# Performance work log

Measured on AMD Instinct MI355X. Metric: run time of the kernel, lower is better.

## Reference

```python
import jax, jax.numpy as jnp
import numpy as np

D_MODEL = 1024
D_STATE = 16
D_CONV = 4
EXPAND = 2
D_INNER = D_MODEL * EXPAND          # 2048
DT_RANK = max(1, D_MODEL // 16)     # 64
BATCH, SEQ = 4, 2048


def setup_inputs() -> dict:
    key = jax.random.key(0)
    ks = jax.random.split(key, 8)
    s = lambda n: 1.0 / np.sqrt(n)
    x = jax.random.normal(ks[0], (BATCH, SEQ, D_MODEL), jnp.float32)
    in_proj_w = jax.random.normal(ks[1], (2 * D_INNER, D_MODEL), jnp.float32) * s(D_MODEL)
    conv_w = jax.random.normal(ks[2], (D_INNER, 1, D_CONV), jnp.float32) * s(D_CONV)
    conv_b = jax.random.normal(ks[3], (D_INNER,), jnp.float32) * 0.01
    x_proj_w = jax.random.normal(ks[4], (DT_RANK + 2 * D_STATE, D_INNER), jnp.float32) * s(D_INNER)
    dt_proj_w = jax.random.normal(ks[5], (D_INNER, DT_RANK), jnp.float32) * s(DT_RANK)
    dt_proj_b = jax.random.normal(ks[6], (D_INNER,), jnp.float32) * 0.01
    A_log = jnp.broadcast_to(jnp.log(jnp.arange(1, D_STATE + 1, dtype=jnp.float32))[None, :],
                             (D_INNER, D_STATE)).copy()
    D_param = jnp.ones((D_INNER,), jnp.float32)
    out_proj_w = jax.random.normal(ks[7], (D_MODEL, D_INNER), jnp.float32) * s(D_INNER)
    return {"x": x, "in_proj_w": in_proj_w, "conv_w": conv_w, "conv_b": conv_b,
            "x_proj_w": x_proj_w, "dt_proj_w": dt_proj_w, "dt_proj_b": dt_proj_b,
            "A_log": A_log, "D_param": D_param, "out_proj_w": out_proj_w}


def _ssm_forward(x, in_proj_w, conv_w, conv_b, x_proj_w, dt_proj_w, dt_proj_b,
                 A_log, D_param, out_proj_w):
    B, L, _ = x.shape
    # input projection -> (B, L, 2*D_INNER), split into x_ssm and gate z
    xz = jnp.einsum('bld,ed->ble', x, in_proj_w)
    x_ssm, z = xz[..., :D_INNER], xz[..., D_INNER:]
    # causal depthwise conv1d (torch pads both sides then slices [:L] == left pad only)
    xc = jnp.transpose(x_ssm, (0, 2, 1))  # (B, D_INNER, L)
    xc = jax.lax.conv_general_dilated(
        xc, conv_w, window_strides=(1,), padding=[(D_CONV - 1, 0)],
        dimension_numbers=('NCH', 'OIH', 'NCH'), feature_group_count=D_INNER)
    xc = xc + conv_b[None, :, None]
    x_ssm = jax.nn.silu(jnp.transpose(xc, (0, 2, 1)))  # (B, L, D_INNER)
    # input-dependent dt, B, C
    dbl = jnp.einsum('bld,ed->ble', x_ssm, x_proj_w)  # (B, L, DT_RANK+2N)
    dt_x = dbl[..., :DT_RANK]
    B_x = dbl[..., DT_RANK:DT_RANK + D_STATE]
    C_x = dbl[..., DT_RANK + D_STATE:]
    dt = jax.nn.softplus(jnp.einsum('blr,dr->bld', dt_x, dt_proj_w) + dt_proj_b)  # (B, L, D_INNER)
    A = -jnp.exp(A_log)  # (D_INNER, D_STATE)

    # selective scan over L with lax.scan; carry h: (B, D_INNER, D_STATE)
    def step(h, inp):
        dt_t, B_t, C_t, x_t = inp  # (B,D), (B,N), (B,N), (B,D)
        dA = jnp.exp(dt_t[:, :, None] * A[None, :, :])          # (B, D, N)
        dB = dt_t[:, :, None] * B_t[:, None, :]                 # (B, D, N)
        h = dA * h + dB * x_t[:, :, None]
        y_t = jnp.einsum('bdn,bn->bd', h, C_t)
        return h, y_t

    h0 = jnp.zeros((B, D_INNER, D_STATE), x.dtype)
    xs = (jnp.moveaxis(dt, 1, 0), jnp.moveaxis(B_x, 1, 0),
          jnp.moveaxis(C_x, 1, 0), jnp.moveaxis(x_ssm, 1, 0))
    _, ys = jax.lax.scan(step, h0, xs)          # ys: (L, B, D_INNER)
    y = jnp.moveaxis(ys, 0, 1) + D_param[None, None, :] * x_ssm
    y = y * jax.nn.silu(z)
    return jnp.einsum('ble,de->bld', y, out_proj_w)


def reference(x, in_proj_w, conv_w, conv_b, x_proj_w, dt_proj_w, dt_proj_b,
              A_log, D_param, out_proj_w):
    return _ssm_forward(x, in_proj_w, conv_w, conv_b, x_proj_w, dt_proj_w,
                        dt_proj_b, A_log, D_param, out_proj_w)
```

## Files before the change

kernel.cpp:

```cpp
#include <hip/hip_runtime.h>
#include <hip/hip_bf16.h>
#include <math.h>

#define D_MODEL 1024
#define D_STATE 16
#define D_CONV 4
#define D_INNER 2048
#define DT_RANK 64
#define BATCH 4
#define SEQ 2048
#define ML (BATCH * SEQ)
#define NCH 64
#define LOG_NCH 6
#define CL (SEQ / NCH)

typedef __attribute__((ext_vector_type(8))) short short8;
typedef __attribute__((ext_vector_type(8))) unsigned short u16x8;
typedef __attribute__((ext_vector_type(4))) float f32x4;

__device__ __forceinline__ float bf2f(unsigned short u) {
  union { unsigned int i; float f; } v;
  v.i = ((unsigned int)u) << 16;
  return v.f;
}
__device__ __forceinline__ unsigned short f2bf(float f) {
  union { float f; unsigned int i; } u;
  u.f = f;
  unsigned int r = u.i + 0x7fffu + ((u.i >> 16) & 1u);
  return (unsigned short)(r >> 16);
}
__device__ __forceinline__ unsigned int f2bf_pk(float a, float b) {
  union { __hip_bfloat162 h; unsigned int u; } cv;
  cv.h = __float22bfloat162_rn(make_float2(a, b));
  return cv.u;
}
template <bool BF>
__device__ __forceinline__ float ld1(const void* p, size_t i) {
  if constexpr (BF) return bf2f(((const unsigned short*)p)[i]);
  else return ((const float*)p)[i];
}
template <bool BF>
__device__ __forceinline__ void ld4(const void* p, size_t i, float o[4]) {
  if constexpr (BF) {
    ushort4 v = *(const ushort4*)((const unsigned short*)p + i);
    o[0] = bf2f(v.x); o[1] = bf2f(v.y); o[2] = bf2f(v.z); o[3] = bf2f(v.w);
  } else {
    float4 v = *(const float4*)((const float*)p + i);
    o[0] = v.x; o[1] = v.y; o[2] = v.z; o[3] = v.w;
  }
}

__device__ __forceinline__ void gl_lds16(const unsigned short* g,
                                         unsigned short* l) {
  __builtin_amdgcn_global_load_lds(
      (const __attribute__((address_space(1))) void*)g,
      (__attribute__((address_space(3))) void*)l, 16, 0, 0);
}

#define CVT_N0 (ML * 1024)
#define CVT_N1 (4096 * 1024)
#define CVT_N2 (1024 * 2048)
#define CVT_N3 (2048 * 64)
#define CVT_N4 (128 * 2048)
#define CVT_E0 CVT_N0
#define CVT_E1 (CVT_E0 + CVT_N1)
#define CVT_E2 (CVT_E1 + CVT_N2)
#define CVT_E3 (CVT_E2 + CVT_N3)
#define CVT_E4 (CVT_E3 + CVT_N4)

__device__ __forceinline__ void cvt4(const void* in, size_t i,
                                     unsigned short* out, size_t o, int bf) {
  if (bf) {
    *(ushort4*)(out + o) = *(const ushort4*)((const unsigned short*)in + i);
  } else {
    float4 f = *(const float4*)((const float*)in + i);
    uint2 v;
    v.x = f2bf_pk(f.x, f.y);
    v.y = f2bf_pk(f.z, f.w);
    *(uint2*)(out + o) = v;
  }
}

__global__ __launch_bounds__(256) void cvt_all_kernel(
    const void* __restrict__ x, const void* __restrict__ ipw,
    const void* __restrict__ opw, const void* __restrict__ dtw,
    const void* __restrict__ xpw, unsigned short* __restrict__ x_bf,
    unsigned short* __restrict__ ipw_bf, unsigned short* __restrict__ opw_bf,
    unsigned short* __restrict__ dtw_bf, unsigned short* __restrict__ xpw_pad,
    int* __restrict__ flag) {
  __shared__ int cnt;
  if (threadIdx.x == 0) cnt = 0;
  __syncthreads();
  {
    const unsigned int wv = ((const unsigned int*)x)[threadIdx.x];
    const unsigned int e = (wv >> 7) & 0xffu;
    if (e < 100u || e > 145u) atomicAdd(&cnt, 1);
  }
  __syncthreads();
  const int bf = (cnt < 32) ? 1 : 0;
  if (blockIdx.x == 0 && threadIdx.x == 0) flag[0] = bf;

  const size_t g = (size_t)(blockIdx.x * 256 + threadIdx.x) * 4;
  if (g < CVT_E0) {
    cvt4(x, g, x_bf, g, bf);
  } else if (g < CVT_E1) {
    const size_t i = g - CVT_E0;
    cvt4(ipw, i, ipw_bf, i, bf);
  } else if (g < CVT_E2) {
    const size_t i = g - CVT_E1;
    cvt4(opw, i, opw_bf, i, bf);
  } else if (g < CVT_E3) {
    const size_t i = g - CVT_E2;
    cvt4(dtw, i, dtw_bf, i, bf);
  } else if (g < CVT_E4) {
    const size_t i = g - CVT_E3;
    const int row = (int)(i >> 11);
    if (row < 96) {
      cvt4(xpw, i, xpw_pad, i, bf);
    } else {
      ushort4 z = {0, 0, 0, 0};
      *(ushort4*)(xpw_pad + i) = z;
    }
  }
}

#define K1_LDA 1024
#define K1_NT 16

#define K1_STG(srcbase, lds, t_, h_)                                       \
  {                                                                        \
    const unsigned short* s_ =                                             \
        (srcbase) + (size_t)(h_) * (128 * K1_LDA) + (size_t)(t_) * 64;     \
    unsigned short* d_ = (lds) + (((t_) & 1) * 2 + (h_)) * 8192 + w * 512; \
    gl_lds16(s_, d_);                                                      \
    gl_lds16(s_ + 64 * K1_LDA, d_ + 4096);                                 \
  }

__global__ __launch_bounds__(512, 2) void gemm256_k1(
    const unsigned short* __restrict__ A,
    const unsigned short* __restrict__ B,
    unsigned short* __restrict__ C) {
  __shared__ unsigned short As[32768];
  __shared__ unsigned short Bs[32768];
  const int tid = threadIdx.x;
  const int l = tid & 63, w = tid >> 6;
  const int bid = blockIdx.x;
  const int swz = (bid & 7) * 64 + (bid >> 3);
  const int m0 = (swz >> 4) * 256, n0 = (swz & 15) * 256;
  const int row0 = tid >> 3;
  const int c0 = (tid & 7) ^ (row0 & 7);
  const unsigned short* aSrc = A + (size_t)(m0 + row0) * K1_LDA + c0 * 8;
  const unsigned short* bSrc = B + (size_t)(n0 + row0) * K1_LDA + c0 * 8;
  const int q = l >> 4, mr = l & 15;
  const int wm = w >> 2, wn = w & 3;

  K1_STG(aSrc, As, 0, 0);
  K1_STG(aSrc, As, 0, 1);
  K1_STG(bSrc, Bs, 0, 0);
  K1_STG(bSrc, Bs, 0, 1);
  K1_STG(bSrc, Bs, 1, 0);
  K1_STG(bSrc, Bs, 1, 1);
  K1_STG(aSrc, As, 1, 0);
  asm volatile("s_waitcnt vmcnt(6)" ::: "memory");
  asm volatile("s_barrier" ::: "memory");

  f32x4 acc[8][4] = {};
  for (int t = 0; t < K1_NT; ++t) {
    const int tb = (t & 1) * 2;
    short8 bfr[4][2];
#pragma unroll
    for (int ni = 0; ni < 4; ++ni)
#pragma unroll
      for (int kk = 0; kk < 2; ++kk) {
        const int r = (wn & 1) * 64 + ni * 16 + mr;
        const int c = kk * 4 + q;
        bfr[ni][kk] = *(const short8*)&Bs[(tb + (wn >> 1)) * 8192 + r * 64 +
                                          ((c ^ (r & 7)) * 8)];
      }
#pragma unroll
    for (int p = 0; p < 4; ++p) {
      short8 af[2][2];
#pragma unroll
      for (int i = 0; i < 2; ++i)
#pragma unroll
        for (int kk = 0; kk < 2; ++kk) {
          const int r = (2 * p + i) * 16 + mr;
          const int c = kk * 4 + q;
          af[i][kk] = *(const short8*)&As[(tb + wm) * 8192 + r * 64 +
                                          ((c ^ (r & 7)) * 8)];
        }
      if (p == 0) {
        if (t + 1 < K1_NT) K1_STG(aSrc, As, t + 1, 1);
      } else if (p == 1) {
        if (t + 2 < K1_NT) K1_STG(bSrc, Bs, t + 2, 0);
      } else if (p == 2) {
        if (t + 2 < K1_NT) K1_STG(bSrc, Bs, t + 2, 1);
      } else {
        if (t + 2 < K1_NT) K1_STG(aSrc, As, t + 2, 0);
      }
      asm volatile("s_barrier" ::: "memory");
      __builtin_amdgcn_s_setprio(1);
#pragma unroll
      for (int i = 0; i < 2; ++i)
#pragma unroll
        for (int ni = 0; ni < 4; ++ni)
#pragma unroll
          for (int kk = 0; kk < 2; ++kk)
            acc[2 * p + i][ni] = __builtin_amdgcn_mfma_f32_16x16x32_bf16(
                af[i][kk], bfr[ni][kk], acc[2 * p + i][ni], 0, 0, 0);
      __builtin_amdgcn_s_setprio(0);
      if (p == 3) {
        if (t + 2 < K1_NT) {
          asm volatile("s_waitcnt vmcnt(6)" ::: "memory");
        } else {
          asm volatile("s_waitcnt vmcnt(0)" ::: "memory");
        }
      }
      asm volatile("s_barrier" ::: "memory");
    }
  }
#pragma unroll
  for (int mi = 0; mi < 8; ++mi) {
#pragma unroll
    for (int ni = 0; ni < 4; ++ni) {
      const int row = m0 + wm * 128 + mi * 16 + q * 4;
      const int col = n0 + wn * 64 + ni * 16 + mr;
      const size_t off0 = (size_t)row * 4096 + col;
      const unsigned int p01 = f2bf_pk(acc[mi][ni][0], acc[mi][ni][1]);
      const unsigned int p23 = f2bf_pk(acc[mi][ni][2], acc[mi][ni][3]);
      C[off0] = (unsigned short)p01;
      C[off0 + 4096] = (unsigned short)(p01 >> 16);
      C[off0 + 2 * 4096] = (unsigned short)p23;
      C[off0 + 3 * 4096] = (unsigned short)(p23 >> 16);
    }
  }
}

#define K6_LDA 2048
#define K6_NT 32

#define K6_STGA(t_, h_)                                                 \
  {                                                                     \
    const unsigned short* s_ =                                          \
        aSrc + (size_t)(h_) * (128 * K6_LDA) + (size_t)(t_) * 64;       \
    unsigned short* d_ = As + (((t_) & 1) * 2 + (h_)) * 8192 + w * 512; \
    gl_lds16(s_, d_);                                                   \
    gl_lds16(s_ + 64 * K6_LDA, d_ + 4096);                              \
  }
#define K6_STGB(t_)                                            \
  {                                                            \
    const unsigned short* s_ = bSrc + (size_t)(t_) * 64;       \
    unsigned short* d_ = Bs6 + ((t_) & 1) * 8192 + w * 512;    \
    gl_lds16(s_, d_);                                          \
    gl_lds16(s_ + 64 * K6_LDA, d_ + 4096);                     \
  }

__global__ __launch_bounds__(512, 2) void gemm256x128_k6(
    const unsigned short* __restrict__ A,
    const unsigned short* __restrict__ B,
    void* __restrict__ C,
    const int* __restrict__ flag) {
  __shared__ unsigned short As[32768];
  __shared__ unsigned short Bs6[16384];
  const int tid = threadIdx.x;
  const int l = tid & 63, w = tid >> 6;
  const int bid = blockIdx.x;
  const int swz = (bid & 7) * 32 + (bid >> 3);
  const int n0 = (swz & 7) * 128, m0 = (swz >> 3) * 256;
  const int row0 = tid >> 3;
  const int c0 = (tid & 7) ^ (row0 & 7);
  const unsigned short* aSrc = A + (size_t)(m0 + row0) * K6_LDA + c0 * 8;
  const unsigned short* bSrc = B + (size_t)(n0 + row0) * K6_LDA + c0 * 8;
  const int q = l >> 4, mr = l & 15;
  const int wm = w >> 2, wn = w & 3;

  K6_STGA(0, 0);
  K6_STGA(0, 1);
  K6_STGB(0);
  K6_STGB(1);
  K6_STGA(1, 0);
  asm volatile("s_waitcnt vmcnt(4)" ::: "memory");
  asm volatile("s_barrier" ::: "memory");

  f32x4 acc[8][2] = {};
  for (int t = 0; t < K6_NT; ++t) {
    const int tb = (t & 1) * 2;
    short8 bfr[2][2];
#pragma unroll
    for (int ni = 0; ni < 2; ++ni)
#pragma unroll
      for (int kk = 0; kk < 2; ++kk) {
        const int r = wn * 32 + ni * 16 + mr;
        const int c = kk * 4 + q;
        bfr[ni][kk] = *(const short8*)&Bs6[(t & 1) * 8192 + r * 64 +
                                           ((c ^ (r & 7)) * 8)];
      }
#pragma unroll
    for (int p = 0; p < 4; ++p) {
      short8 af[2][2];
#pragma unroll
      for (int i = 0; i < 2; ++i)
#pragma unroll
        for (int kk = 0; kk < 2; ++kk) {
          const int r = (2 * p + i) * 16 + mr;
          const int c = kk * 4 + q;
          af[i][kk] = *(const short8*)&As[(tb + wm) * 8192 + r * 64 +
                                          ((c ^ (r & 7)) * 8)];
        }
      if (p == 0) {
        if (t + 1 < K6_NT) K6_STGA(t + 1, 1);
      } else if (p == 1) {
        if (t + 2 < K6_NT) K6_STGB(t + 2);
      } else if (p == 3) {
        if (t + 2 < K6_NT) K6_STGA(t + 2, 0);
      }
      asm volatile("s_barrier" ::: "memory");
      __builtin_amdgcn_s_setprio(1);
#pragma unroll
      for (int i = 0; i < 2; ++i)
#pragma unroll
        for (int ni = 0; ni < 2; ++ni)
#pragma unroll
          for (int kk = 0; kk < 2; ++kk)
            acc[2 * p + i][ni] = __builtin_amdgcn_mfma_f32_16x16x32_bf16(
                af[i][kk], bfr[ni][kk], acc[2 * p + i][ni], 0, 0, 0);
      __builtin_amdgcn_s_setprio(0);
      if (p == 3) {
        if (t + 2 < K6_NT) {
          asm volatile("s_waitcnt vmcnt(4)" ::: "memory");
        } else {
          asm volatile("s_waitcnt vmcnt(0)" ::: "memory");
        }
      }
      asm volatile("s_barrier" ::: "memory");
    }
  }
  const int bf = *flag;
#pragma unroll
  for (int mi = 0; mi < 8; ++mi) {
#pragma unroll
    for (int ni = 0; ni < 2; ++ni) {
      const int row = m0 + wm * 128 + mi * 16 + q * 4;
      const int col = n0 + wn * 32 + ni * 16 + mr;
      const size_t off0 = (size_t)row * 1024 + col;
      if (bf) {
        const unsigned int p01 = f2bf_pk(acc[mi][ni][0], acc[mi][ni][1]);
        const unsigned int p23 = f2bf_pk(acc[mi][ni][2], acc[mi][ni][3]);
        unsigned short* C16 = (unsigned short*)C;
        C16[off0] = (unsigned short)p01;
        C16[off0 + 1024] = (unsigned short)(p01 >> 16);
        C16[off0 + 2 * 1024] = (unsigned short)p23;
        C16[off0 + 3 * 1024] = (unsigned short)(p23 >> 16);
      } else {
        float* Cf = (float*)C;
#pragma unroll
        for (int j = 0; j < 4; ++j)
          Cf[off0 + (size_t)j * 1024] = acc[mi][ni][j];
      }
    }
  }
}

template <int EPI, int TAG>
__global__ __launch_bounds__(256) void gemm_mfma(
    const unsigned short* __restrict__ Ain, int lda,
    const unsigned short* __restrict__ Bin, int ldb, void* __restrict__ C,
    int ldc, int K, const void* __restrict__ bias,
    const int* __restrict__ flag) {
  __shared__ unsigned short As[128 * 32];
  __shared__ unsigned short Bs[128 * 32];
  const unsigned short* A = Ain;
  const unsigned short* B = Bin;
  if (EPI == 3) {
    A += (size_t)blockIdx.z * 512;
    B += (size_t)blockIdx.z * 512;
  }
  const int tid = threadIdx.x;
  const int l = tid & 63, w = tid >> 6;
  const int bm = blockIdx.y * 128;
  const int bn = blockIdx.x * 128;
  const int r0 = w * 16 + (l >> 2);
  const int cc = (((l & 3) ^ ((l >> 2) & 3) ^ ((l >> 4) & 3))) * 8;
  const unsigned short* Ap0 = A + (size_t)(bm + r0) * lda + cc;
  const unsigned short* Ap1 = A + (size_t)(bm + r0 + 64) * lda + cc;
  const unsigned short* Bp0 = B + (size_t)(bn + r0) * ldb + cc;
  const unsigned short* Bp1 = B + (size_t)(bn + r0 + 64) * ldb + cc;
  const int q = l >> 4, mr = l & 15;
  const int wm = w >> 1, wn = w & 1;
  const int slot = (q ^ (mr & 3) ^ (mr >> 2)) * 8;
  f32x4 acc[4][4] = {};
  for (int k0 = 0; k0 < K; k0 += 32) {
    gl_lds16(Ap0 + k0, As + w * 512);
    gl_lds16(Ap1 + k0, As + 2048 + w * 512);
    gl_lds16(Bp0 + k0, Bs + w * 512);
    gl_lds16(Bp1 + k0, Bs + 2048 + w * 512);
    __syncthreads();
    short8 af[4], bfr[4];
#pragma unroll
    for (int mi = 0; mi < 4; ++mi)
      af[mi] = *(const short8*)&As[(wm * 64 + mi * 16 + mr) * 32 + slot];
#pragma unroll
    for (int ni = 0; ni < 4; ++ni)
      bfr[ni] = *(const short8*)&Bs[(wn * 64 + ni * 16 + mr) * 32 + slot];
#pragma unroll
    for (int mi = 0; mi < 4; ++mi)
#pragma unroll
      for (int ni = 0; ni < 4; ++ni)
        acc[mi][ni] = __builtin_amdgcn_mfma_f32_16x16x32_bf16(
            af[mi], bfr[ni], acc[mi][ni], 0, 0, 0);
    __syncthreads();
  }
  float* Cp3 = (EPI == 3)
                   ? ((float*)C + (size_t)blockIdx.z * ML * 128)
                   : (float*)C;
#pragma unroll
  for (int mi = 0; mi < 4; ++mi) {
#pragma unroll
    for (int ni = 0; ni < 4; ++ni) {
      const int row = bm + wm * 64 + mi * 16 + q * 4;
      const int col = bn + wn * 64 + ni * 16 + mr;
      const size_t off0 = (size_t)row * ldc + col;
      if (EPI == 3) {
#pragma unroll
        for (int j = 0; j < 4; ++j)
          Cp3[off0 + (size_t)j * ldc] = acc[mi][ni][j];
      } else {
        const unsigned int p01 = f2bf_pk(acc[mi][ni][0], acc[mi][ni][1]);
        const unsigned int p23 = f2bf_pk(acc[mi][ni][2], acc[mi][ni][3]);
        unsigned short* C16 = (unsigned short*)C;
        C16[off0] = (unsigned short)p01;
        C16[off0 + ldc] = (unsigned short)(p01 >> 16);
        C16[off0 + 2 * (size_t)ldc] = (unsigned short)p23;
        C16[off0 + 3 * (size_t)ldc] = (unsigned short)(p23 >> 16);
      }
    }
  }
}

__global__ __launch_bounds__(256) void reduceK3_kernel(
    const float* __restrict__ part, unsigned short* __restrict__ dbl) {
  const size_t i = (size_t)(blockIdx.x * 256 + threadIdx.x) * 4;
  const size_t st = (size_t)ML * 128;
  float4 a = *(const float4*)(part + i);
  float4 b = *(const float4*)(part + st + i);
  float4 c = *(const float4*)(part + 2 * st + i);
  float4 d = *(const float4*)(part + 3 * st + i);
  uint2 v;
  v.x = f2bf_pk(a.x + b.x + c.x + d.x, a.y + b.y + c.y + d.y);
  v.y = f2bf_pk(a.z + b.z + c.z + d.z, a.w + b.w + c.w + d.w);
  *(uint2*)(dbl + i) = v;
}

__global__ __launch_bounds__(256) void dt_gemm_kernel(
    const unsigned short* __restrict__ Adbl,
    const unsigned short* __restrict__ Bw,
    unsigned short* __restrict__ Cdt,
    const void* __restrict__ bias, const int* __restrict__ flag) {
  __shared__ unsigned short Bs[128 * 64];
  __shared__ unsigned short Ass[4][128 * 64];
  const int tid = threadIdx.x;
  const int l = tid & 63, w = tid >> 6;
  const int bn = blockIdx.x * 128;
  const int mg = blockIdx.y * 512;
  const int srow = tid >> 3;
  const int sc = ((tid & 7) ^ (srow & 7)) * 8;
  const unsigned short* aSrc = Adbl + (size_t)(mg + srow) * 128 + sc;
  const unsigned short* bSrc = Bw + (size_t)(bn + srow) * 64 + sc;
#define K4_STGB(i_) gl_lds16(bSrc + (i_) * 32 * 64, Bs + (i_)*2048 + w * 512)
#define K4_STGA(mt_, i_)                                  \
  gl_lds16(aSrc + (size_t)((mt_)*128 + (i_)*32) * 128,    \
           Ass[(mt_) & 3] + (i_)*2048 + w * 512)
  K4_STGB(0); K4_STGB(1); K4_STGB(2); K4_STGB(3);
  K4_STGA(0, 0); K4_STGA(0, 1); K4_STGA(0, 2); K4_STGA(0, 3);
  K4_STGA(1, 0); K4_STGA(1, 1); K4_STGA(1, 2); K4_STGA(1, 3);
  asm volatile("s_waitcnt vmcnt(4)" ::: "memory");
  asm volatile("s_barrier" ::: "memory");
  const int q = l >> 4, mr = l & 15;
  const int wm = w >> 1, wn = w & 1;
  short8 bfr[4][2];
#pragma unroll
  for (int ni = 0; ni < 4; ++ni)
#pragma unroll
    for (int kk = 0; kk < 2; ++kk) {
      const int r = wn * 64 + ni * 16 + mr;
      const int c = kk * 4 + q;
      bfr[ni][kk] = *(const short8*)&Bs[r * 64 + ((c ^ (r & 7)) * 8)];
    }
  const int bf = *flag;
  float bv[4];
#pragma unroll
  for (int ni = 0; ni < 4; ++ni) {
    const int col = bn + wn * 64 + ni * 16 + mr;
    bv[ni] = bf ? ld1<true>(bias, col) : ld1<false>(bias, col);
  }
#pragma unroll
  for (int mt = 0; mt < 4; ++mt) {
    if (mt + 2 < 4) {
      K4_STGA(mt + 2, 0); K4_STGA(mt + 2, 1);
      K4_STGA(mt + 2, 2); K4_STGA(mt + 2, 3);
    }
    short8 af[4][2];
#pragma unroll
    for (int mi = 0; mi < 4; ++mi)
#pragma unroll
      for (int kk = 0; kk < 2; ++kk) {
        const int r = wm * 64 + mi * 16 + mr;
        const int c = kk * 4 + q;
        af[mi][kk] =
            *(const short8*)&Ass[mt & 3][r * 64 + ((c ^ (r & 7)) * 8)];
      }
    f32x4 acc[4][4] = {};
#pragma unroll
    for (int mi = 0; mi < 4; ++mi)
#pragma unroll
      for (int ni = 0; ni < 4; ++ni)
#pragma unroll
        for (int kk = 0; kk < 2; ++kk)
          acc[mi][ni] = __builtin_amdgcn_mfma_f32_16x16x32_bf16(
              af[mi][kk], bfr[ni][kk], acc[mi][ni], 0, 0, 0);
#pragma unroll
    for (int mi = 0; mi < 4; ++mi) {
#pragma unroll
      for (int ni = 0; ni < 4; ++ni) {
        const int row = mg + mt * 128 + wm * 64 + mi * 16 + q * 4;
        const int col = bn + wn * 64 + ni * 16 + mr;
        const size_t off0 = (size_t)row * 4096 + col;
        float v[4];
#pragma unroll
        for (int j = 0; j < 4; ++j) {
          const float t = acc[mi][ni][j] + bv[ni];
          v[j] = fmaxf(t, 0.f) + __logf(1.f + __expf(-fabsf(t)));
        }
        const unsigned int p01 = f2bf_pk(v[0], v[1]);
        const unsigned int p23 = f2bf_pk(v[2], v[3]);
        Cdt[off0] = (unsigned short)p01;
        Cdt[off0 + 4096] = (unsigned short)(p01 >> 16);
        Cdt[off0 + 2 * 4096] = (unsigned short)p23;
        Cdt[off0 + 3 * 4096] = (unsigned short)(p23 >> 16);
      }
    }
    if (mt + 2 < 4) {
      asm volatile("s_waitcnt vmcnt(4)" ::: "memory");
    } else {
      asm volatile("s_waitcnt vmcnt(0)" ::: "memory");
    }
    if (mt < 3) asm volatile("s_barrier" ::: "memory");
  }
}

__global__ __launch_bounds__(256) void conv_silu_kernel(
    const unsigned short* __restrict__ xzb, const void* __restrict__ cw,
    const void* __restrict__ cb, unsigned short* __restrict__ xcb,
    const int* __restrict__ flag) {
  const int bf = *flag;
  const int e = (blockIdx.x * 256 + threadIdx.x) * 4;
  const int d = e & (D_INNER - 1);
  const int bl = e >> 11;
  const int l = bl & (SEQ - 1);
  const size_t base = (size_t)bl * 4096 + d;
  float x0[4], x1[4] = {}, x2[4] = {}, x3[4] = {};
  ld4<true>(xzb, base, x0);
  if (l >= 1) ld4<true>(xzb, base - 4096, x1);
  if (l >= 2) ld4<true>(xzb, base - 2 * 4096, x2);
  if (l >= 3) ld4<true>(xzb, base - 3 * 4096, x3);
  float r[4];
#pragma unroll
  for (int i = 0; i < 4; ++i) {
    float w[4];
    if (bf) ld4<true>(cw, (size_t)(d + i) * 4, w);
    else ld4<false>(cw, (size_t)(d + i) * 4, w);
    const float bias = bf ? ld1<true>(cb, d + i) : ld1<false>(cb, d + i);
    float acc = bias + w[3] * x0[i] + w[2] * x1[i] + w[1] * x2[i] + w[0] * x3[i];
    r[i] = acc / (1.f + __expf(-acc));
  }
  uint2 o;
  o.x = f2bf_pk(r[0], r[1]);
  o.y = f2bf_pk(r[2], r[3]);
  *(uint2*)(xcb + e) = o;
}

__device__ __forceinline__ void load_a(const void* A_log, int bf, int d,
                                       float a[16], float& dev) {
  float t[4];
#pragma unroll
  for (int k = 0; k < 4; ++k) {
    if (bf) ld4<true>(A_log, (size_t)d * 16 + k * 4, t);
    else ld4<false>(A_log, (size_t)d * 16 + k * 4, t);
#pragma unroll
    for (int j = 0; j < 4; ++j) a[k * 4 + j] = -expf(t[j]);
  }
  dev = 0.f;
#pragma unroll
  for (int n = 0; n < 16; ++n) dev = fmaxf(dev, fabsf(a[n] + (float)(n + 1)));
}

__device__ __forceinline__ void pow_tree(float e1, float pw[16]) {
  const float e2 = e1 * e1;
  const float e3 = e2 * e1;
  const float e4 = e2 * e2;
  pw[0] = e1; pw[1] = e2; pw[2] = e3; pw[3] = e4;
  pw[4] = e4 * e1; pw[5] = e4 * e2; pw[6] = e4 * e3; pw[7] = e4 * e4;
  const float e8 = pw[7];
  pw[8] = e8 * e1; pw[9] = e8 * e2; pw[10] = e8 * e3; pw[11] = e8 * e4;
  pw[12] = e8 * pw[4]; pw[13] = e8 * pw[5]; pw[14] = e8 * pw[6];
  pw[15] = e8 * e8;
}

__global__ __launch_bounds__(256) void scan_passA(
    const unsigned short* __restrict__ xzb,
    const unsigned short* __restrict__ xcb,
    const unsigned short* __restrict__ dbl, const void* __restrict__ A_log,
    const int* __restrict__ flag, float* __restrict__ S,
    float* __restrict__ Sdt) {
  const int bf = *flag;
  const int gid = blockIdx.x * 256 + threadIdx.x;
  const int d = gid & (D_INNER - 1);
  const int c = (gid >> 11) & (NCH - 1);
  const int b = gid >> (11 + LOG_NCH);
  float a[16], dev;
  load_a(A_log, bf, d, a, dev);
  float h[16] = {};
  float sdt = 0.f;
  const size_t m0 = (size_t)b * SEQ + c * CL;
  if (dev < 1e-3f) {
    for (int t = 0; t < CL; ++t) {
      const size_t m = m0 + t;
      const float dtv = bf2f(xzb[m * 4096 + d]);
      const float xv = bf2f(xcb[m * 2048 + d]);
      const u16x8 B0 = *(const u16x8*)&dbl[m * 128 + 64];
      const u16x8 B1 = *(const u16x8*)&dbl[m * 128 + 72];
      const float dtx = dtv * xv;
      sdt += dtv;
      float pw[16];
      pow_tree(__expf(-dtv), pw);
#pragma unroll
      for (int n = 0; n < 16; ++n) {
        const float Bv = bf2f(n < 8 ? B0[n] : B1[n - 8]);
        h[n] = fmaf(pw[n], h[n], Bv * dtx);
      }
    }
  } else {
    for (int t = 0; t < CL; ++t) {
      const size_t m = m0 + t;
      const float dtv = bf2f(xzb[m * 4096 + d]);
      const float xv = bf2f(xcb[m * 2048 + d]);
      const u16x8 B0 = *(const u16x8*)&dbl[m * 128 + 64];
      const u16x8 B1 = *(const u16x8*)&dbl[m * 128 + 72];
      const float dtx = dtv * xv;
      sdt += dtv;
#pragma unroll
      for (int n = 0; n < 16; ++n) {
        const float Bv = bf2f(n < 8 ? B0[n] : B1[n - 8]);
        h[n] = fmaf(__expf(dtv * a[n]), h[n], Bv * dtx);
      }
    }
  }
  const size_t sbase = (((size_t)b * NCH + c) * 16) * D_INNER + d;
#pragma unroll
  for (int n = 0; n < 16; ++n) S[sbase + (size_t)n * D_INNER] = h[n];
  Sdt[((size_t)b * NCH + c) * D_INNER + d] = sdt;
}

__global__ __launch_bounds__(256) void scan_passB(
    float* __restrict__ S, const float* __restrict__ Sdt,
    const void* __restrict__ A_log, const int* __restrict__ flag) {
  const int bf = *flag;
  const int idx = blockIdx.x * 256 + threadIdx.x;
  const int d = idx & (D_INNER - 1);
  const int n = (idx >> 11) & 15;
  const int b = idx >> 15;
  const float al = bf ? ld1<true>(A_log, (size_t)d * 16 + n)
                      : ld1<false>(A_log, (size_t)d * 16 + n);
  const float a = -expf(al);
  float h = 0.f;
  for (int c = 0; c < NCH; ++c) {
    const size_t base = ((size_t)b * NCH + c);
    const size_t sidx = (base * 16 + n) * D_INNER + d;
    const float s = S[sidx];
    const float sdt = Sdt[base * D_INNER + d];
    const float p = __expf(a * sdt);
    S[sidx] = h;
    h = p * h + s;
  }
}

__global__ __launch_bounds__(256) void scan_passC(
    const unsigned short* __restrict__ xzb,
    const unsigned short* __restrict__ xcb,
    const unsigned short* __restrict__ dbl, const void* __restrict__ A_log,
    const void* __restrict__ Dp, const float* __restrict__ S,
    const int* __restrict__ flag, unsigned short* __restrict__ ybf) {
  const int bf = *flag;
  const int gid = blockIdx.x * 256 + threadIdx.x;
  const int d = gid & (D_INNER - 1);
  const int c = (gid >> 11) & (NCH - 1);
  const int b = gid >> (11 + LOG_NCH);
  float a[16], dev;
  load_a(A_log, bf, d, a, dev);
  const float Dv = bf ? ld1<true>(Dp, d) : ld1<false>(Dp, d);
  float h[16];
  const size_t sbase = (((size_t)b * NCH + c) * 16) * D_INNER + d;
#pragma unroll
  for (int n = 0; n < 16; ++n) h[n] = S[sbase + (size_t)n * D_INNER];
  const size_t m0 = (size_t)b * SEQ + c * CL;
  const bool trick = dev < 1e-3f;
  for (int t = 0; t < CL; ++t) {
    const size_t m = m0 + t;
    const float dtv = bf2f(xzb[m * 4096 + d]);
    const float xv = bf2f(xcb[m * 2048 + d]);
    const u16x8 B0 = *(const u16x8*)&dbl[m * 128 + 64];
    const u16x8 B1 = *(const u16x8*)&dbl[m * 128 + 72];
    const u16x8 C0 = *(const u16x8*)&dbl[m * 128 + 80];
    const u16x8 C1 = *(const u16x8*)&dbl[m * 128 + 88];
    const float dtx = dtv * xv;
    float y = 0.f;
    if (trick) {
      float pw[16];
      pow_tree(__expf(-dtv), pw);
#pragma unroll
      for (int n = 0; n < 16; ++n) {
        const float Bv = bf2f(n < 8 ? B0[n] : B1[n - 8]);
        const float Cv = bf2f(n < 8 ? C0[n] : C1[n - 8]);
        h[n] = fmaf(pw[n], h[n], Bv * dtx);
        y = fmaf(h[n], Cv, y);
      }
    } else {
#pragma unroll
      for (int n = 0; n < 16; ++n) {
        const float Bv = bf2f(n < 8 ? B0[n] : B1[n - 8]);
        const float Cv = bf2f(n < 8 ? C0[n] : C1[n - 8]);
        h[n] = fmaf(__expf(dtv * a[n]), h[n], Bv * dtx);
        y = fmaf(h[n], Cv, y);
      }
    }
    const float zv = bf2f(xzb[m * 4096 + 2048 + d]);
    const float yv = y + Dv * xv;
    ybf[m * 2048 + d] = f2bf(yv * (zv / (1.f + __expf(-zv))));
  }
}

extern "C" void kernel_launch(void* const* d_in, const int* in_sizes, int n_in,
                              void* d_out, int out_size, void* d_ws,
                              size_t ws_size, hipStream_t stream) {
  const void* x = d_in[0];
  const void* in_proj_w = d_in[1];
  const void* conv_w = d_in[2];
  const void* conv_b = d_in[3];
  const void* x_proj_w = d_in[4];
  const void* dt_proj_w = d_in[5];
  const void* dt_proj_b = d_in[6];
  const void* A_log = d_in[7];
  const void* D_param = d_in[8];
  const void* out_proj_w = d_in[9];

  char* wsb = (char*)d_ws;
  int* flag = (int*)wsb;
  unsigned short* xzb = (unsigned short*)(wsb + 256);
  unsigned short* xcb = xzb + (size_t)ML * 4096;
  unsigned short* dbl = xcb + (size_t)ML * 2048;
  unsigned short* ybf = dbl + (size_t)ML * 128;
  float* S = (float*)(ybf + (size_t)ML * 2048);
  float* Sdt = S + (size_t)BATCH * NCH * D_INNER * 16;
  unsigned short* opw_bf =
      (unsigned short*)(Sdt + (size_t)BATCH * NCH * D_INNER);
  unsigned short* xpw_pad = opw_bf + (size_t)1024 * 2048;
  unsigned short* dtw_bf = xpw_pad + (size_t)128 * 2048;
  unsigned short* x_bf = xcb;
  unsigned short* ipw_bf = xcb + (size_t)ML * 1024;
  float* k3part = S;

  cvt_all_kernel<<<CVT_E4 / 1024, 256, 0, stream>>>(
      x, in_proj_w, out_proj_w, dt_proj_w, x_proj_w, x_bf, ipw_bf, opw_bf,
      dtw_bf, xpw_pad, flag);
  gemm256_k1<<<dim3(512), 512, 0, stream>>>(x_bf, ipw_bf, xzb);
  conv_silu_kernel<<<(ML * D_INNER) / 1024, 256, 0, stream>>>(
      xzb, conv_w, conv_b, xcb, flag);
  {
    dim3 g(1, ML / 128, 4);
    gemm_mfma<3, 3><<<g, 256, 0, stream>>>(xcb, 2048, xpw_pad, 2048, k3part,
                                           128, 512, nullptr, flag);
  }
  reduceK3_kernel<<<(ML * 128) / 1024, 256, 0, stream>>>(k3part, dbl);
  dt_gemm_kernel<<<dim3(16, 16), 256, 0, stream>>>(dbl, dtw_bf, xzb,
                                                   dt_proj_b, flag);
  scan_passA<<<(BATCH * NCH * D_INNER) / 256, 256, 0, stream>>>(
      xzb, xcb, dbl, A_log, flag, S, Sdt);
  scan_passB<<<(BATCH * D_INNER * 16) / 256, 256, 0, stream>>>(S, Sdt, A_log,
                                                               flag);
  scan_passC<<<(BATCH * NCH * D_INNER) / 256, 256, 0, stream>>>(
      xzb, xcb, dbl, A_log, D_param, S, flag, ybf);
  gemm256x128_k6<<<dim3(256), 512, 0, stream>>>(ybf, opw_bf, d_out, flag);
}
```

Measured before the change: 438.7 us.

## Split scan state dimension across two half-waves per channel

Scan passes A and C now assign two lanes to each channel, each handling 8 of the 16 state entries. Pass C combines the two partial outputs with a cross-lane shuffle, and the grid doubles to keep the same channel coverage. The aim is more threads in flight and shorter serial dependency chains with fewer registers per thread. In exchange, each block covers only 128 channels, the dt, x and z loads are repeated across both halves, and half the lanes sit idle for the output store.

```diff
diff --git a/kernel.cpp b/kernel.cpp
--- a/kernel.cpp
+++ b/kernel.cpp
@@ -579,31 +579,36 @@
   *(uint2*)(xcb + e) = o;
 }
 
-__device__ __forceinline__ void load_a(const void* A_log, int bf, int d,
-                                       float a[16], float& dev) {
-  float t[4];
-#pragma unroll
-  for (int k = 0; k < 4; ++k) {
-    if (bf) ld4<true>(A_log, (size_t)d * 16 + k * 4, t);
-    else ld4<false>(A_log, (size_t)d * 16 + k * 4, t);
-#pragma unroll
-    for (int j = 0; j < 4; ++j) a[k * 4 + j] = -expf(t[j]);
+__device__ __forceinline__ void load_a8(const void* A_log, int bf, int d,
+                                        int half, float a[8], float& dev) {
+  float t0[4], t1[4];
+  const size_t off = (size_t)d * 16 + half * 8;
+  if (bf) {
+    ld4<true>(A_log, off, t0);
+    ld4<true>(A_log, off + 4, t1);
+  } else {
+    ld4<false>(A_log, off, t0);
+    ld4<false>(A_log, off + 4, t1);
+  }
+#pragma unroll
+  for (int j = 0; j < 4; ++j) {
+    a[j] = -expf(t0[j]);
+    a[4 + j] = -expf(t1[j]);
   }
   dev = 0.f;
 #pragma unroll
-  for (int n = 0; n < 16; ++n) dev = fmaxf(dev, fabsf(a[n] + (float)(n + 1)));
-}
-
-__device__ __forceinline__ void pow_tree(float e1, float pw[16]) {
+  for (int j = 0; j < 8; ++j)
+    dev = fmaxf(dev, fabsf(a[j] + (float)(half * 8 + j + 1)));
+}
+
+__device__ __forceinline__ void pow8(float e1, int half, float pw[8]) {
   const float e2 = e1 * e1;
   const float e3 = e2 * e1;
   const float e4 = e2 * e2;
-  pw[0] = e1; pw[1] = e2; pw[2] = e3; pw[3] = e4;
-  pw[4] = e4 * e1; pw[5] = e4 * e2; pw[6] = e4 * e3; pw[7] = e4 * e4;
-  const float e8 = pw[7];
-  pw[8] = e8 * e1; pw[9] = e8 * e2; pw[10] = e8 * e3; pw[11] = e8 * e4;
-  pw[12] = e8 * pw[4]; pw[13] = e8 * pw[5]; pw[14] = e8 * pw[6];
-  pw[15] = e8 * e8;
+  const float e5 = e4 * e1, e6 = e4 * e2, e7 = e4 * e3, e8 = e4 * e4;
+  const float s = half ? e8 : 1.0f;
+  pw[0] = s * e1; pw[1] = s * e2; pw[2] = s * e3; pw[3] = s * e4;
+  pw[4] = s * e5; pw[5] = s * e6; pw[6] = s * e7; pw[7] = s * e8;
 }
 
 __global__ __launch_bounds__(256) void scan_passA(
@@ -613,52 +618,51 @@
     const int* __restrict__ flag, float* __restrict__ S,
     float* __restrict__ Sdt) {
   const int bf = *flag;
-  const int gid = blockIdx.x * 256 + threadIdx.x;
-  const int d = gid & (D_INNER - 1);
-  const int c = (gid >> 11) & (NCH - 1);
-  const int b = gid >> (11 + LOG_NCH);
-  float a[16], dev;
-  load_a(A_log, bf, d, a, dev);
-  float h[16] = {};
+  const int blk = blockIdx.x;
+  const int tid = threadIdx.x;
+  const int lane = tid & 63, w = tid >> 6;
+  const int half = lane >> 5, dl = lane & 31;
+  const int d = ((blk & 15) << 7) + w * 32 + dl;
+  const int c = (blk >> 4) & (NCH - 1);
+  const int b = blk >> (4 + LOG_NCH);
+  float a[8], dev;
+  load_a8(A_log, bf, d, half, a, dev);
+  const bool trick = dev < 1e-3f;
+  float h[8] = {};
   float sdt = 0.f;
   const size_t m0 = (size_t)b * SEQ + c * CL;
-  if (dev < 1e-3f) {
+  if (trick) {
     for (int t = 0; t < CL; ++t) {
       const size_t m = m0 + t;
       const float dtv = bf2f(xzb[m * 4096 + d]);
       const float xv = bf2f(xcb[m * 2048 + d]);
-      const u16x8 B0 = *(const u16x8*)&dbl[m * 128 + 64];
-      const u16x8 B1 = *(const u16x8*)&dbl[m * 128 + 72];
+      const u16x8 Bv = *(const u16x8*)&dbl[m * 128 + 64 + half * 8];
       const float dtx = dtv * xv;
       sdt += dtv;
-      float pw[16];
-      pow_tree(__expf(-dtv), pw);
-#pragma unroll
-      for (int n = 0; n < 16; ++n) {
-        const float Bv = bf2f(n < 8 ? B0[n] : B1[n - 8]);
-        h[n] = fmaf(pw[n], h[n], Bv * dtx);
-      }
+      float pw[8];
+      pow8(__expf(-dtv), half, pw);
+#pragma unroll
+      for (int n = 0; n < 8; ++n)
+        h[n] = fmaf(pw[n], h[n], bf2f(Bv[n]) * dtx);
     }
   } else {
     for (int t = 0; t < CL; ++t) {
       const size_t m = m0 + t;
       const float dtv = bf2f(xzb[m * 4096 + d]);
       const float xv = bf2f(xcb[m * 2048 + d]);
-      const u16x8 B0 = *(const u16x8*)&dbl[m * 128 + 64];
-      const u16x8 B1 = *(const u16x8*)&dbl[m * 128 + 72];
+      const u16x8 Bv = *(const u16x8*)&dbl[m * 128 + 64 + half * 8];
       const float dtx = dtv * xv;
       sdt += dtv;
 #pragma unroll
-      for (int n = 0; n < 16; ++n) {
-        const float Bv = bf2f(n < 8 ? B0[n] : B1[n - 8]);
-        h[n] = fmaf(__expf(dtv * a[n]), h[n], Bv * dtx);
-      }
-    }
-  }
-  const size_t sbase = (((size_t)b * NCH + c) * 16) * D_INNER + d;
-#pragma unroll
-  for (int n = 0; n < 16; ++n) S[sbase + (size_t)n * D_INNER] = h[n];
-  Sdt[((size_t)b * NCH + c) * D_INNER + d] = sdt;
+      for (int n = 0; n < 8; ++n)
+        h[n] = fmaf(__expf(dtv * a[n]), h[n], bf2f(Bv[n]) * dtx);
+    }
+  }
+  const size_t sbase =
+      (((size_t)b * NCH + c) * 16 + half * 8) * D_INNER + d;
+#pragma unroll
+  for (int n = 0; n < 8; ++n) S[sbase + (size_t)n * D_INNER] = h[n];
+  if (!half) Sdt[((size_t)b * NCH + c) * D_INNER + d] = sdt;
 }
 
 __global__ __launch_bounds__(256) void scan_passB(
@@ -691,51 +695,52 @@
     const void* __restrict__ Dp, const float* __restrict__ S,
     const int* __restrict__ flag, unsigned short* __restrict__ ybf) {
   const int bf = *flag;
-  const int gid = blockIdx.x * 256 + threadIdx.x;
-  const int d = gid & (D_INNER - 1);
-  const int c = (gid >> 11) & (NCH - 1);
-  const int b = gid >> (11 + LOG_NCH);
-  float a[16], dev;
-  load_a(A_log, bf, d, a, dev);
+  const int blk = blockIdx.x;
+  const int tid = threadIdx.x;
+  const int lane = tid & 63, w = tid >> 6;
+  const int half = lane >> 5, dl = lane & 31;
+  const int d = ((blk & 15) << 7) + w * 32 + dl;
+  const int c = (blk >> 4) & (NCH - 1);
+  const int b = blk >> (4 + LOG_NCH);
+  float a[8], dev;
+  load_a8(A_log, bf, d, half, a, dev);
+  const bool trick = dev < 1e-3f;
   const float Dv = bf ? ld1<true>(Dp, d) : ld1<false>(Dp, d);
-  float h[16];
-  const size_t sbase = (((size_t)b * NCH + c) * 16) * D_INNER + d;
-#pragma unroll
-  for (int n = 0; n < 16; ++n) h[n] = S[sbase + (size_t)n * D_INNER];
+  float h[8];
+  const size_t sbase =
+      (((size_t)b * NCH + c) * 16 + half * 8) * D_INNER + d;
+#pragma unroll
+  for (int n = 0; n < 8; ++n) h[n] = S[sbase + (size_t)n * D_INNER];
   const size_t m0 = (size_t)b * SEQ + c * CL;
-  const bool trick = dev < 1e-3f;
   for (int t = 0; t < CL; ++t) {
     const size_t m = m0 + t;
     const float dtv = bf2f(xzb[m * 4096 + d]);
     const float xv = bf2f(xcb[m * 2048 + d]);
-    const u16x8 B0 = *(const u16x8*)&dbl[m * 128 + 64];
-    const u16x8 B1 = *(const u16x8*)&dbl[m * 128 + 72];
-    const u16x8 C0 = *(const u16x8*)&dbl[m * 128 + 80];
-    const u16x8 C1 = *(const u16x8*)&dbl[m * 128 + 88];
+    const u16x8 Bv = *(const u16x8*)&dbl[m * 128 + 64 + half * 8];
+    const u16x8 Cv = *(const u16x8*)&dbl[m * 128 + 80 + half * 8];
     const float dtx = dtv * xv;
     float y = 0.f;
     if (trick) {
-      float pw[16];
-      pow_tree(__expf(-dtv), pw);
-#pragma unroll
-      for (int n = 0; n < 16; ++n) {
-        const float Bv = bf2f(n < 8 ? B0[n] : B1[n - 8]);
-        const float Cv = bf2f(n < 8 ? C0[n] : C1[n - 8]);
-        h[n] = fmaf(pw[n], h[n], Bv * dtx);
-        y = fmaf(h[n], Cv, y);
+      float pw[8];
+      pow8(__expf(-dtv), half, pw);
+#pragma unroll
+      for (int n = 0; n < 8; ++n) {
+        h[n] = fmaf(pw[n], h[n], bf2f(Bv[n]) * dtx);
+        y = fmaf(h[n], bf2f(Cv[n]), y);
       }
     } else {
 #pragma unroll
-      for (int n = 0; n < 16; ++n) {
-        const float Bv = bf2f(n < 8 ? B0[n] : B1[n - 8]);
-        const float Cv = bf2f(n < 8 ? C0[n] : C1[n - 8]);
-        h[n] = fmaf(__expf(dtv * a[n]), h[n], Bv * dtx);
-        y = fmaf(h[n], Cv, y);
-      }
-    }
-    const float zv = bf2f(xzb[m * 4096 + 2048 + d]);
-    const float yv = y + Dv * xv;
-    ybf[m * 2048 + d] = f2bf(yv * (zv / (1.f + __expf(-zv))));
+      for (int n = 0; n < 8; ++n) {
+        h[n] = fmaf(__expf(dtv * a[n]), h[n], bf2f(Bv[n]) * dtx);
+        y = fmaf(h[n], bf2f(Cv[n]), y);
+      }
+    }
+    y += __shfl_xor(y, 32);
+    if (!half) {
+      const float zv = bf2f(xzb[m * 4096 + 2048 + d]);
+      const float yv = y + Dv * xv;
+      ybf[m * 2048 + d] = f2bf(yv * (zv / (1.f + __expf(-zv))));
+    }
   }
 }
 
@@ -783,11 +788,11 @@
   reduceK3_kernel<<<(ML * 128) / 1024, 256, 0, stream>>>(k3part, dbl);
   dt_gemm_kernel<<<dim3(16, 16), 256, 0, stream>>>(dbl, dtw_bf, xzb,
                                                    dt_proj_b, flag);
-  scan_passA<<<(BATCH * NCH * D_INNER) / 256, 256, 0, stream>>>(
+  scan_passA<<<BATCH * NCH * (D_INNER / 128), 256, 0, stream>>>(
       xzb, xcb, dbl, A_log, flag, S, Sdt);
   scan_passB<<<(BATCH * D_INNER * 16) / 256, 256, 0, stream>>>(S, Sdt, A_log,
                                                                flag);
-  scan_passC<<<(BATCH * NCH * D_INNER) / 256, 256, 0, stream>>>(
+  scan_passC<<<BATCH * NCH * (D_INNER / 128), 256, 0, stream>>>(
       xzb, xcb, dbl, A_log, D_param, S, flag, ybf);
   gemm256x128_k6<<<dim3(256), 512, 0, stream>>>(ybf, opw_bf, d_out, flag);
 }
```

Result: slower. 466.4 us (+6.3%).
